# Performance work log

Measured on AMD Instinct MI355X. Metric: run time of the kernel, lower is better.

Reference implementation:

```python
import jax, jax.numpy as jnp
import numpy as np

DIM = 1024
NUM_HEADS = 16
HEAD_DIM = DIM // NUM_HEADS


def setup_inputs() -> dict:
    key = jax.random.key(0)
    k1, k2, k3, k4, k5 = jax.random.split(key, 5)
    B, N = 4, 2048
    x = jax.random.normal(k1, (B, N, DIM), dtype=jnp.float32)
    s_in = 1.0 / np.sqrt(DIM)
    W_qkv = jax.random.normal(k2, (DIM, 3 * DIM), dtype=jnp.float32) * s_in
    b_qkv = jax.random.normal(k3, (3 * DIM,), dtype=jnp.float32) * 0.02
    W_proj = jax.random.normal(k4, (DIM, DIM), dtype=jnp.float32) * s_in
    b_proj = jax.random.normal(k5, (DIM,), dtype=jnp.float32) * 0.02
    return {"x": x, "W_qkv": W_qkv, "b_qkv": b_qkv, "W_proj": W_proj, "b_proj": b_proj}


def reference(x, W_qkv, b_qkv, W_proj, b_proj):
    B, N, C = x.shape
    H, D = NUM_HEADS, HEAD_DIM
    scale = D ** -0.5
    qkv = x @ W_qkv + b_qkv                      # [B, N, 3C]
    qkv = qkv.reshape(B, N, 3, H, D)
    q = jnp.transpose(qkv[:, :, 0], (0, 2, 1, 3))  # [B, H, N, D]
    k = jnp.transpose(qkv[:, :, 1], (0, 2, 1, 3))
    v = jnp.transpose(qkv[:, :, 2], (0, 2, 1, 3))
    # scaled dot-product attention (dropout_p=0 in eval)
    attn = jnp.einsum("bhqd,bhkd->bhqk", q, k) * scale
    attn = jax.nn.softmax(attn, axis=-1)
    o = jnp.einsum("bhqk,bhkd->bhqd", attn, v)   # [B, H, N, D]
    o = jnp.transpose(o, (0, 2, 1, 3)).reshape(B, N, C)
    return o @ W_proj + b_proj
```

## Files before the change

### kernel.cpp

```cpp
#include <hip/hip_runtime.h>
#include <hip/hip_bf16.h>
#include <cstdint>

#define DIMC 1024
#define NHEAD 16
#define HD 64
#define SEQ 2048
#define NTOK 8192

typedef __attribute__((ext_vector_type(8))) short bfrag;
typedef __attribute__((ext_vector_type(4))) short spack4;
typedef __attribute__((ext_vector_type(4))) float fv4;
typedef __attribute__((ext_vector_type(16))) float f32x16;
typedef __attribute__((ext_vector_type(4))) int iv4;

static __device__ __forceinline__ unsigned short f2bf(float f) {
  union { float f; unsigned int u; } v; v.f = f;
  return (unsigned short)((v.u + 0x7fffu + ((v.u >> 16) & 1u)) >> 16);
}
static __device__ __forceinline__ unsigned int pack2c(float a, float b) {
  __hip_bfloat16 ha(a), hb(b);
  unsigned short ua, ub;
  __builtin_memcpy(&ua, &ha, 2);
  __builtin_memcpy(&ub, &hb, 2);
  return (unsigned int)ua | ((unsigned int)ub << 16);
}

#define MFMA(a, b, c) __builtin_amdgcn_mfma_f32_16x16x32_bf16((a), (b), (c), 0, 0, 0)
#define MFMA32(a, b, c) __builtin_amdgcn_mfma_f32_32x32x16_bf16((a), (b), (c), 0, 0, 0)

#define GLOAD_LDS(gp, lp)                                                  \
  __builtin_amdgcn_global_load_lds(                                        \
      (const __attribute__((address_space(1))) void*)(gp),                 \
      (__attribute__((address_space(3))) void*)(lp), 16, 0, 0)

__global__ void cvt_x(const float* __restrict__ x, short* __restrict__ xb) {
  int i = (blockIdx.x * 256 + threadIdx.x) * 4;
  fv4 v = *(const fv4*)&x[i];
  spack4 o;
#pragma unroll
  for (int j = 0; j < 4; ++j) o[j] = (short)f2bf(v[j]);
  *(spack4*)&xb[i] = o;
}

__global__ void transpose_w(const float* __restrict__ W, short* __restrict__ WT,
                            int R, int C) {
  __shared__ float tile[32][33];
  const int t = threadIdx.x;
  const int r = t >> 3, c4 = t & 7;
  const int r0 = blockIdx.y * 32, c0 = blockIdx.x * 32;
  fv4 v = *(const fv4*)&W[(size_t)(r0 + r) * C + c0 + c4 * 4];
#pragma unroll
  for (int j = 0; j < 4; ++j) tile[r][c4 * 4 + j] = v[j];
  __syncthreads();
  spack4 o;
#pragma unroll
  for (int j = 0; j < 4; ++j) o[j] = (short)f2bf(tile[c4 * 4 + j][r]);
  *(spack4*)&WT[(size_t)(c0 + r) * R + r0 + c4 * 4] = o;
}

template <int MODE>
__launch_bounds__(256)
__global__ void gemm_bt(const short* __restrict__ A, const short* __restrict__ BT,
                        const float* __restrict__ bias, int M, int N, int K,
                        short* __restrict__ out0, short* __restrict__ out1,
                        short* __restrict__ out2, float* __restrict__ outf) {
  __shared__ alignas(16) char As[128 * 128];
  __shared__ alignas(16) char Bs[128 * 128];
  const int t = threadIdx.x;
  const int lane = t & 63;
  const int wid = t >> 6;
  const int wm = wid >> 1, wn = wid & 1;
  const int g = lane >> 4, l15 = lane & 15;
  const int row0 = blockIdx.y * 128;
  const int col0 = blockIdx.x * 128;

  fv4 acc[4][4] = {};

  const int srow = t >> 3;
  const int sk = (((t & 7) ^ (srow & 7)) * 8);

  for (int k0 = 0; k0 < K; k0 += 64) {
#pragma unroll
    for (int i = 0; i < 4; ++i) {
      const int row = i * 32 + srow;
      GLOAD_LDS(&A[(size_t)(row0 + row) * K + k0 + sk], &As[i * 4096 + t * 16]);
      GLOAD_LDS(&BT[(size_t)(col0 + row) * K + k0 + sk], &Bs[i * 4096 + t * 16]);
    }
    __syncthreads();
#pragma unroll
    for (int kk = 0; kk < 2; ++kk) {
      bfrag af[4], bf[4];
#pragma unroll
      for (int mm = 0; mm < 4; ++mm) {
        int row = wm * 64 + mm * 16 + l15;
        af[mm] = *(const bfrag*)&As[row * 128 + ((kk * 64 + g * 16) ^ ((row & 7) << 4))];
      }
#pragma unroll
      for (int nn = 0; nn < 4; ++nn) {
        int row = wn * 64 + nn * 16 + l15;
        bf[nn] = *(const bfrag*)&Bs[row * 128 + ((kk * 64 + g * 16) ^ ((row & 7) << 4))];
      }
#pragma unroll
      for (int mm = 0; mm < 4; ++mm)
#pragma unroll
        for (int nn = 0; nn < 4; ++nn)
          acc[mm][nn] = MFMA(af[mm], bf[nn], acc[mm][nn]);
    }
    __syncthreads();
  }

  if (MODE == 0) {
    const float qs = 0.125f * 1.4426950408889634f;
#pragma unroll
    for (int nn = 0; nn < 4; ++nn) {
      int col = col0 + wn * 64 + nn * 16 + l15;
      int which = col >> 10;
      int rem = col & 1023;
      int h = rem >> 6, d = rem & 63;
      float bval = bias[col];
#pragma unroll
      for (int mm = 0; mm < 4; ++mm) {
        int tok = row0 + wm * 64 + mm * 16 + g * 4;
        int b = tok >> 11, n = tok & 2047;
        int bh = b * NHEAD + h;
        if (which == 0) {
#pragma unroll
          for (int r = 0; r < 4; ++r)
            out0[((size_t)bh * SEQ + n + r) * HD + d] =
                (short)f2bf((acc[mm][nn][r] + bval) * qs);
        } else if (which == 1) {
#pragma unroll
          for (int r = 0; r < 4; ++r)
            out1[((size_t)bh * SEQ + n + r) * HD + d] =
                (short)f2bf(acc[mm][nn][r] + bval);
        } else {
          int n2 = (n & ~15) | ((n & 4) << 1) | ((n & 8) >> 1);
          spack4 p;
#pragma unroll
          for (int r = 0; r < 4; ++r) p[r] = (short)f2bf(acc[mm][nn][r] + bval);
          *(spack4*)&out2[((size_t)bh * HD + d) * SEQ + n2] = p;
        }
      }
    }
  } else {
#pragma unroll
    for (int nn = 0; nn < 4; ++nn) {
      int col = col0 + wn * 64 + nn * 16 + l15;
      float bval = bias[col];
#pragma unroll
      for (int mm = 0; mm < 4; ++mm) {
        int tok = row0 + wm * 64 + mm * 16 + g * 4;
#pragma unroll
        for (int r = 0; r < 4; ++r)
          outf[(size_t)(tok + r) * N + col] = acc[mm][nn][r] + bval;
      }
    }
  }
}

__launch_bounds__(256, 2)
__global__ void attn_fwd(const short* __restrict__ Q, const short* __restrict__ Kb,
                         const short* __restrict__ VT, short* __restrict__ O) {
  __shared__ alignas(16) char Ks[2][8192];
  __shared__ alignas(16) char Vs[2][8192];

  const int t = threadIdx.x, lane = t & 63, wid = t >> 6;
  const int l31 = lane & 31, hi = lane >> 5;
  const int rsw = (l31 & 7) << 4;

  const int bid = blockIdx.x;
  const int xcd = bid & 7, mm_ = bid >> 3;
  const int bh = xcd + 8 * (mm_ >> 3);
  const int qt = mm_ & 7;

  const size_t base = (size_t)bh * SEQ * HD;
  const short* Qp = Q + base;
  const short* Kp = Kb + base;
  const short* Vp = VT + base;
  const int q0 = qt * 256 + wid * 32;
  const int q1 = q0 + 128;

  bfrag qfA[4], qfB[4];
#pragma unroll
  for (int dblk = 0; dblk < 4; ++dblk) {
    qfA[dblk] = *(const bfrag*)&Qp[(size_t)(q0 + l31) * HD + dblk * 16 + hi * 8];
    qfB[dblk] = *(const bfrag*)&Qp[(size_t)(q1 + l31) * HD + dblk * 16 + hi * 8];
  }

  f32x16 oaccA[2] = {}, oaccB[2] = {};
  float lA = 0.f, lB = 0.f;

  const int sr = t >> 3, ss = t & 7;
  const int swz0 = (ss * 16) ^ ((sr & 7) << 4);

  {
    bfrag k0 = *(const bfrag*)&Kp[(size_t)sr * HD + ss * 8];
    bfrag k1 = *(const bfrag*)&Kp[(size_t)(32 + sr) * HD + ss * 8];
    bfrag v0 = *(const bfrag*)&Vp[(size_t)sr * SEQ + ss * 8];
    bfrag v1 = *(const bfrag*)&Vp[(size_t)(sr + 32) * SEQ + ss * 8];
    *(bfrag*)&Ks[0][sr * 128 + swz0] = k0;
    *(bfrag*)&Ks[0][(sr + 32) * 128 + swz0] = k1;
    *(bfrag*)&Vs[0][sr * 128 + swz0] = v0;
    *(bfrag*)&Vs[0][(sr + 32) * 128 + swz0] = v1;
  }
  __syncthreads();

  int cur = 0;
  for (int kt = 0; kt < SEQ / 64; ++kt) {
    bfrag nk0, nk1, nv0, nv1;
    const bool pre = (kt + 1) < (SEQ / 64);
    if (pre) {
      const int kb2 = (kt + 1) * 64;
      nk0 = *(const bfrag*)&Kp[(size_t)(kb2 + sr) * HD + ss * 8];
      nk1 = *(const bfrag*)&Kp[(size_t)(kb2 + 32 + sr) * HD + ss * 8];
      nv0 = *(const bfrag*)&Vp[(size_t)sr * SEQ + kb2 + ss * 8];
      nv1 = *(const bfrag*)&Vp[(size_t)(sr + 32) * SEQ + kb2 + ss * 8];
    }

    const char* Kc = Ks[cur];
    const char* Vc = Vs[cur];

    f32x16 sA0 = {}, sA1 = {}, sB0 = {}, sB1 = {};
    __builtin_amdgcn_s_setprio(1);
#pragma unroll
    for (int dblk = 0; dblk < 4; ++dblk) {
      const int c = (dblk * 32 + hi * 16) ^ rsw;
      bfrag kf0 = *(const bfrag*)&Kc[l31 * 128 + c];
      bfrag kf1 = *(const bfrag*)&Kc[(32 + l31) * 128 + c];
      sA0 = MFMA32(kf0, qfA[dblk], sA0);
      sB0 = MFMA32(kf0, qfB[dblk], sB0);
      sA1 = MFMA32(kf1, qfA[dblk], sA1);
      sB1 = MFMA32(kf1, qfB[dblk], sB1);
    }
    __builtin_amdgcn_s_setprio(0);

    unsigned int pwA0[8], pwA1[8], pwB0[8], pwB1[8];
    float sumA = 0.f, sumB = 0.f;
#define PACK8(sv, pw, sum)                                   \
  _Pragma("unroll")                                          \
  for (int i = 0; i < 8; ++i) {                              \
    float e0 = __builtin_amdgcn_exp2f(sv[2 * i]);            \
    float e1 = __builtin_amdgcn_exp2f(sv[2 * i + 1]);        \
    sum += e0 + e1;                                          \
    pw[i] = pack2c(e0, e1);                                  \
  }
    PACK8(sA0, pwA0, sumA)
    PACK8(sA1, pwA1, sumA)
    PACK8(sB0, pwB0, sumB)
    PACK8(sB1, pwB1, sumB)
#undef PACK8
    lA += sumA + __shfl_xor(sumA, 32);
    lB += sumB + __shfl_xor(sumB, 32);

    __builtin_amdgcn_s_setprio(1);
#define PV_HB(hb, WA, WB)                                                   \
  {                                                                         \
    const int o4 = ((hb) & 1) * 4;                                          \
    iv4 ia = { (int)WA[o4], (int)WA[o4 + 1], (int)WA[o4 + 2], (int)WA[o4 + 3] }; \
    iv4 ib = { (int)WB[o4], (int)WB[o4 + 1], (int)WB[o4 + 2], (int)WB[o4 + 3] }; \
    const bfrag pbA = __builtin_bit_cast(bfrag, ia);                        \
    const bfrag pbB = __builtin_bit_cast(bfrag, ib);                        \
    _Pragma("unroll")                                                       \
    for (int dh = 0; dh < 2; ++dh) {                                        \
      const int row = dh * 32 + l31;                                        \
      bfrag vf = *(const bfrag*)&Vc[row * 128 + (((hb) * 32 + hi * 16) ^ rsw)]; \
      oaccA[dh] = MFMA32(vf, pbA, oaccA[dh]);                               \
      oaccB[dh] = MFMA32(vf, pbB, oaccB[dh]);                               \
    }                                                                       \
  }
    PV_HB(0, pwA0, pwB0)
    PV_HB(1, pwA0, pwB0)
    PV_HB(2, pwA1, pwB1)
    PV_HB(3, pwA1, pwB1)
#undef PV_HB
    __builtin_amdgcn_s_setprio(0);

    if (pre) {
      const int nb = cur ^ 1;
      *(bfrag*)&Ks[nb][sr * 128 + swz0] = nk0;
      *(bfrag*)&Ks[nb][(sr + 32) * 128 + swz0] = nk1;
      *(bfrag*)&Vs[nb][sr * 128 + swz0] = nv0;
      *(bfrag*)&Vs[nb][(sr + 32) * 128 + swz0] = nv1;
      __syncthreads();
    }
    cur ^= 1;
  }

  const float invA = 1.0f / lA;
  const float invB = 1.0f / lB;
  const int b = bh >> 4, h = bh & 15;
#pragma unroll
  for (int dh = 0; dh < 2; ++dh)
#pragma unroll
    for (int gp = 0; gp < 4; ++gp) {
      const int d0 = dh * 32 + gp * 8 + hi * 4;
      spack4 pkA, pkB;
#pragma unroll
      for (int j = 0; j < 4; ++j) {
        pkA[j] = (short)f2bf(oaccA[dh][gp * 4 + j] * invA);
        pkB[j] = (short)f2bf(oaccB[dh][gp * 4 + j] * invB);
      }
      *(spack4*)&O[((size_t)b * SEQ + (q0 + l31)) * DIMC + h * HD + d0] = pkA;
      *(spack4*)&O[((size_t)b * SEQ + (q1 + l31)) * DIMC + h * HD + d0] = pkB;
    }
}

extern "C" void kernel_launch(void* const* d_in, const int* in_sizes, int n_in,
                              void* d_out, int out_size, void* d_ws, size_t ws_size,
                              hipStream_t stream) {
  const float* x     = (const float*)d_in[0];
  const float* Wqkv  = (const float*)d_in[1];
  const float* bqkv  = (const float*)d_in[2];
  const float* Wproj = (const float*)d_in[3];
  const float* bproj = (const float*)d_in[4];
  float* out = (float*)d_out;
  char* ws = (char*)d_ws;

  short* xb  = (short*)(ws);
  short* WqT = (short*)(ws + 16777216);
  short* WpT = (short*)(ws + 23068672);
  short* Qb  = (short*)(ws + 25165824);
  short* Kb  = (short*)(ws + 41943040);
  short* VTb = (short*)(ws + 58720256);
  short* Ob  = (short*)(ws + 75497472);

  cvt_x<<<8192, 256, 0, stream>>>(x, xb);
  transpose_w<<<dim3(96, 32), 256, 0, stream>>>(Wqkv, WqT, 1024, 3072);
  transpose_w<<<dim3(32, 32), 256, 0, stream>>>(Wproj, WpT, 1024, 1024);
  gemm_bt<0><<<dim3(24, 64), 256, 0, stream>>>(xb, WqT, bqkv, NTOK, 3072, 1024,
                                               Qb, Kb, VTb, nullptr);
  attn_fwd<<<512, 256, 0, stream>>>(Qb, Kb, VTb, Ob);
  gemm_bt<1><<<dim3(8, 64), 256, 0, stream>>>(Ob, WpT, bproj, NTOK, 1024, 1024,
                                              nullptr, nullptr, nullptr, out);
}
```

Baseline: 190.4 us.

## Fuse prep kernels into one launch and double attention KV tile to 128

Merges the x conversion and both weight transposes into a single prep kernel selected by block index, removing two kernel launches. In attention, each iteration now stages a 128-key K/V tile (two 64-key halves processed in sequence) instead of 64, halving the number of __syncthreads barriers and LDS refills per sequence. This doubles LDS use to 64KB per block and raises the registers needed to hold prefetched data, which may affect the two-blocks-per-CU occupancy.

Measured after the change: 206.8 us. 1.09x slower.

```diff
diff --git a/kernel.cpp b/kernel.cpp
--- a/kernel.cpp
+++ b/kernel.cpp
@@ -34,21 +34,28 @@
       (const __attribute__((address_space(1))) void*)(gp),                 \
       (__attribute__((address_space(3))) void*)(lp), 16, 0, 0)
 
-__global__ void cvt_x(const float* __restrict__ x, short* __restrict__ xb) {
-  int i = (blockIdx.x * 256 + threadIdx.x) * 4;
-  fv4 v = *(const fv4*)&x[i];
-  spack4 o;
-#pragma unroll
-  for (int j = 0; j < 4; ++j) o[j] = (short)f2bf(v[j]);
-  *(spack4*)&xb[i] = o;
-}
-
-__global__ void transpose_w(const float* __restrict__ W, short* __restrict__ WT,
-                            int R, int C) {
+__global__ void prep(const float* __restrict__ x, short* __restrict__ xb,
+                     const float* __restrict__ Wqkv, short* __restrict__ WqT,
+                     const float* __restrict__ Wproj, short* __restrict__ WpT) {
   __shared__ float tile[32][33];
+  const int bid = blockIdx.x;
   const int t = threadIdx.x;
+  if (bid < 8192) {
+    int i = (bid * 256 + t) * 4;
+    fv4 v = *(const fv4*)&x[i];
+    spack4 o;
+#pragma unroll
+    for (int j = 0; j < 4; ++j) o[j] = (short)f2bf(v[j]);
+    *(spack4*)&xb[i] = o;
+    return;
+  }
+  const float* W; short* WT; int R, C, bx, by;
+  if (bid < 11264) { W = Wqkv; WT = WqT; R = 1024; C = 3072;
+                     bx = (bid - 8192) % 96; by = (bid - 8192) / 96; }
+  else             { W = Wproj; WT = WpT; R = 1024; C = 1024;
+                     bx = (bid - 11264) % 32; by = (bid - 11264) / 32; }
   const int r = t >> 3, c4 = t & 7;
-  const int r0 = blockIdx.y * 32, c0 = blockIdx.x * 32;
+  const int r0 = by * 32, c0 = bx * 32;
   fv4 v = *(const fv4*)&W[(size_t)(r0 + r) * C + c0 + c4 * 4];
 #pragma unroll
   for (int j = 0; j < 4; ++j) tile[r][c4 * 4 + j] = v[j];
@@ -162,8 +169,8 @@
 __launch_bounds__(256, 2)
 __global__ void attn_fwd(const short* __restrict__ Q, const short* __restrict__ Kb,
                          const short* __restrict__ VT, short* __restrict__ O) {
-  __shared__ alignas(16) char Ks[2][8192];
-  __shared__ alignas(16) char Vs[2][8192];
+  __shared__ alignas(16) char Ks[2][16384];
+  __shared__ alignas(16) char Vs[2][16384];
 
   const int t = threadIdx.x, lane = t & 63, wid = t >> 6;
   const int l31 = lane & 31, hi = lane >> 5;
@@ -192,51 +199,59 @@
   float lA = 0.f, lB = 0.f;
 
   const int sr = t >> 3, ss = t & 7;
-  const int swz0 = (ss * 16) ^ ((sr & 7) << 4);
+  const int swzK = (ss * 16) ^ ((sr & 7) << 4);
+  const int vr = t >> 2, vs = t & 3;
 
   {
-    bfrag k0 = *(const bfrag*)&Kp[(size_t)sr * HD + ss * 8];
-    bfrag k1 = *(const bfrag*)&Kp[(size_t)(32 + sr) * HD + ss * 8];
-    bfrag v0 = *(const bfrag*)&Vp[(size_t)sr * SEQ + ss * 8];
-    bfrag v1 = *(const bfrag*)&Vp[(size_t)(sr + 32) * SEQ + ss * 8];
-    *(bfrag*)&Ks[0][sr * 128 + swz0] = k0;
-    *(bfrag*)&Ks[0][(sr + 32) * 128 + swz0] = k1;
-    *(bfrag*)&Vs[0][sr * 128 + swz0] = v0;
-    *(bfrag*)&Vs[0][(sr + 32) * 128 + swz0] = v1;
+#pragma unroll
+    for (int i = 0; i < 4; ++i) {
+      bfrag kv = *(const bfrag*)&Kp[(size_t)(sr + 32 * i) * HD + ss * 8];
+      *(bfrag*)&Ks[0][(sr + 32 * i) * 128 + swzK] = kv;
+    }
+#pragma unroll
+    for (int j = 0; j < 4; ++j) {
+      const int c = vs + 4 * j;
+      bfrag vv = *(const bfrag*)&Vp[(size_t)vr * SEQ + c * 8];
+      *(bfrag*)&Vs[0][vr * 256 + ((c * 16) ^ ((vr & 7) << 4))] = vv;
+    }
   }
   __syncthreads();
 
   int cur = 0;
-  for (int kt = 0; kt < SEQ / 64; ++kt) {
-    bfrag nk0, nk1, nv0, nv1;
-    const bool pre = (kt + 1) < (SEQ / 64);
+  for (int kt = 0; kt < SEQ / 128; ++kt) {
+    bfrag nk[4], nv[4];
+    const bool pre = (kt + 1) < (SEQ / 128);
     if (pre) {
-      const int kb2 = (kt + 1) * 64;
-      nk0 = *(const bfrag*)&Kp[(size_t)(kb2 + sr) * HD + ss * 8];
-      nk1 = *(const bfrag*)&Kp[(size_t)(kb2 + 32 + sr) * HD + ss * 8];
-      nv0 = *(const bfrag*)&Vp[(size_t)sr * SEQ + kb2 + ss * 8];
-      nv1 = *(const bfrag*)&Vp[(size_t)(sr + 32) * SEQ + kb2 + ss * 8];
+      const int kb2 = (kt + 1) * 128;
+#pragma unroll
+      for (int i = 0; i < 4; ++i)
+        nk[i] = *(const bfrag*)&Kp[(size_t)(kb2 + sr + 32 * i) * HD + ss * 8];
+#pragma unroll
+      for (int j = 0; j < 4; ++j)
+        nv[j] = *(const bfrag*)&Vp[(size_t)vr * SEQ + kb2 + (vs + 4 * j) * 8];
     }
 
     const char* Kc = Ks[cur];
     const char* Vc = Vs[cur];
 
-    f32x16 sA0 = {}, sA1 = {}, sB0 = {}, sB1 = {};
-    __builtin_amdgcn_s_setprio(1);
-#pragma unroll
-    for (int dblk = 0; dblk < 4; ++dblk) {
-      const int c = (dblk * 32 + hi * 16) ^ rsw;
-      bfrag kf0 = *(const bfrag*)&Kc[l31 * 128 + c];
-      bfrag kf1 = *(const bfrag*)&Kc[(32 + l31) * 128 + c];
-      sA0 = MFMA32(kf0, qfA[dblk], sA0);
-      sB0 = MFMA32(kf0, qfB[dblk], sB0);
-      sA1 = MFMA32(kf1, qfA[dblk], sA1);
-      sB1 = MFMA32(kf1, qfB[dblk], sB1);
-    }
-    __builtin_amdgcn_s_setprio(0);
-
-    unsigned int pwA0[8], pwA1[8], pwB0[8], pwB1[8];
-    float sumA = 0.f, sumB = 0.f;
+#pragma unroll
+    for (int h = 0; h < 2; ++h) {
+      f32x16 sA0 = {}, sA1 = {}, sB0 = {}, sB1 = {};
+      __builtin_amdgcn_s_setprio(1);
+#pragma unroll
+      for (int dblk = 0; dblk < 4; ++dblk) {
+        const int c = (dblk * 32 + hi * 16) ^ rsw;
+        bfrag kf0 = *(const bfrag*)&Kc[(h * 64 + l31) * 128 + c];
+        bfrag kf1 = *(const bfrag*)&Kc[(h * 64 + 32 + l31) * 128 + c];
+        sA0 = MFMA32(kf0, qfA[dblk], sA0);
+        sB0 = MFMA32(kf0, qfB[dblk], sB0);
+        sA1 = MFMA32(kf1, qfA[dblk], sA1);
+        sB1 = MFMA32(kf1, qfB[dblk], sB1);
+      }
+      __builtin_amdgcn_s_setprio(0);
+
+      unsigned int pwA0[8], pwA1[8], pwB0[8], pwB1[8];
+      float sumA = 0.f, sumB = 0.f;
 #define PACK8(sv, pw, sum)                                   \
   _Pragma("unroll")                                          \
   for (int i = 0; i < 8; ++i) {                              \
@@ -245,15 +260,15 @@
     sum += e0 + e1;                                          \
     pw[i] = pack2c(e0, e1);                                  \
   }
-    PACK8(sA0, pwA0, sumA)
-    PACK8(sA1, pwA1, sumA)
-    PACK8(sB0, pwB0, sumB)
-    PACK8(sB1, pwB1, sumB)
+      PACK8(sA0, pwA0, sumA)
+      PACK8(sA1, pwA1, sumA)
+      PACK8(sB0, pwB0, sumB)
+      PACK8(sB1, pwB1, sumB)
 #undef PACK8
-    lA += sumA + __shfl_xor(sumA, 32);
-    lB += sumB + __shfl_xor(sumB, 32);
-
-    __builtin_amdgcn_s_setprio(1);
+      lA += sumA + __shfl_xor(sumA, 32);
+      lB += sumB + __shfl_xor(sumB, 32);
+
+      __builtin_amdgcn_s_setprio(1);
 #define PV_HB(hb, WA, WB)                                                   \
   {                                                                         \
     const int o4 = ((hb) & 1) * 4;                                          \
@@ -264,24 +279,30 @@
     _Pragma("unroll")                                                       \
     for (int dh = 0; dh < 2; ++dh) {                                        \
       const int row = dh * 32 + l31;                                        \
-      bfrag vf = *(const bfrag*)&Vc[row * 128 + (((hb) * 32 + hi * 16) ^ rsw)]; \
+      bfrag vf = *(const bfrag*)&Vc[row * 256 +                             \
+                   ((h * 128 + (hb) * 32 + hi * 16) ^ rsw)];                \
       oaccA[dh] = MFMA32(vf, pbA, oaccA[dh]);                               \
       oaccB[dh] = MFMA32(vf, pbB, oaccB[dh]);                               \
     }                                                                       \
   }
-    PV_HB(0, pwA0, pwB0)
-    PV_HB(1, pwA0, pwB0)
-    PV_HB(2, pwA1, pwB1)
-    PV_HB(3, pwA1, pwB1)
+      PV_HB(0, pwA0, pwB0)
+      PV_HB(1, pwA0, pwB0)
+      PV_HB(2, pwA1, pwB1)
+      PV_HB(3, pwA1, pwB1)
 #undef PV_HB
-    __builtin_amdgcn_s_setprio(0);
+      __builtin_amdgcn_s_setprio(0);
+    }
 
     if (pre) {
       const int nb = cur ^ 1;
-      *(bfrag*)&Ks[nb][sr * 128 + swz0] = nk0;
-      *(bfrag*)&Ks[nb][(sr + 32) * 128 + swz0] = nk1;
-      *(bfrag*)&Vs[nb][sr * 128 + swz0] = nv0;
-      *(bfrag*)&Vs[nb][(sr + 32) * 128 + swz0] = nv1;
+#pragma unroll
+      for (int i = 0; i < 4; ++i)
+        *(bfrag*)&Ks[nb][(sr + 32 * i) * 128 + swzK] = nk[i];
+#pragma unroll
+      for (int j = 0; j < 4; ++j) {
+        const int c = vs + 4 * j;
+        *(bfrag*)&Vs[nb][vr * 256 + ((c * 16) ^ ((vr & 7) << 4))] = nv[j];
+      }
       __syncthreads();
     }
     cur ^= 1;
@@ -325,9 +346,7 @@
   short* VTb = (short*)(ws + 58720256);
   short* Ob  = (short*)(ws + 75497472);
 
-  cvt_x<<<8192, 256, 0, stream>>>(x, xb);
-  transpose_w<<<dim3(96, 32), 256, 0, stream>>>(Wqkv, WqT, 1024, 3072);
-  transpose_w<<<dim3(32, 32), 256, 0, stream>>>(Wproj, WpT, 1024, 1024);
+  prep<<<12288, 256, 0, stream>>>(x, xb, Wqkv, WqT, Wproj, WpT);
   gemm_bt<0><<<dim3(24, 64), 256, 0, stream>>>(xb, WqT, bqkv, NTOK, 3072, 1024,
                                                Qb, Kb, VTb, nullptr);
   attn_fwd<<<512, 256, 0, stream>>>(Qb, Kb, VTb, Ob);
```
